# Kernel optimization log

Hardware: AMD Instinct MI355X
Metric: run time of the kernel (lower is better)

The kernel has to match this reference:

```python
import jax, jax.numpy as jnp
import numpy as np
import math

NUM_HEADS = 6
HIDDEN = 384
HEAD_CH = HIDDEN // NUM_HEADS
WINDOW = 4


def _get_relative_embeddings(emb, length, window):
    # emb: (H, 2*window+1, d) -> (H, 2*length-1, d)
    pad_length = max(0, length - window - 1)
    start = max(0, window - length + 1)
    padded = jnp.pad(emb, ((0, 0), (pad_length, pad_length), (0, 0)))
    return padded[:, start:start + 2 * length - 1, :]


def _relative_to_absolute(s_rel):
    # (B, H, L, 2L-1) -> (B, H, L, L) via shift-pad trick
    B, H, L, _ = s_rel.shape
    s = jnp.pad(s_rel, ((0, 0), (0, 0), (0, 0), (0, 1)))          # (B,H,L,2L)
    s = s.reshape(B, H, L * 2 * L)
    s = jnp.pad(s, ((0, 0), (0, 0), (0, L - 1)))
    s = s.reshape(B, H, L + 1, 2 * L - 1)
    return s[:, :, :L, L - 1:]


def _absolute_to_relative(score):
    # (B, H, L, L) -> (B, H, L, 2L-1)
    B, H, L, _ = score.shape
    s = jnp.pad(score, ((0, 0), (0, 0), (0, 0), (0, L - 1)))      # (B,H,L,2L-1)
    s = s.reshape(B, H, L * (2 * L - 1))
    s = jnp.pad(s, ((0, 0), (0, 0), (L, 0)))
    s = s.reshape(B, H, L, 2 * L)
    return s[:, :, :, 1:]


def setup_inputs() -> dict:
    key = jax.random.key(0)
    ks = jax.random.split(key, 11)
    B, C, L = 8, HIDDEN, 1024
    rel_std = HEAD_CH ** -0.5
    w_std = C ** -0.5
    return {
        "x": jax.random.normal(ks[0], (B, C, L), jnp.float32),
        "wq": jax.random.normal(ks[1], (C, C), jnp.float32) * w_std,
        "bq": jax.random.normal(ks[2], (C,), jnp.float32) * 0.01,
        "wk": jax.random.normal(ks[3], (C, C), jnp.float32) * w_std,
        "bk": jax.random.normal(ks[4], (C,), jnp.float32) * 0.01,
        "wv": jax.random.normal(ks[5], (C, C), jnp.float32) * w_std,
        "bv": jax.random.normal(ks[6], (C,), jnp.float32) * 0.01,
        "wo": jax.random.normal(ks[7], (C, C), jnp.float32) * w_std,
        "bo": jax.random.normal(ks[8], (C,), jnp.float32) * 0.01,
        "emb_rel_k": jax.random.normal(ks[9], (NUM_HEADS, 2 * WINDOW + 1, HEAD_CH), jnp.float32) * rel_std,
        "emb_rel_v": jax.random.normal(ks[10], (NUM_HEADS, 2 * WINDOW + 1, HEAD_CH), jnp.float32) * rel_std,
    }


def reference(x, wq, bq, wk, bk, wv, bv, wo, bo, emb_rel_k, emb_rel_v):
    B, C, L = x.shape
    H, d = NUM_HEADS, HEAD_CH
    scale = 1.0 / math.sqrt(d)

    # 1x1 convs == channel matmuls
    q = jnp.einsum('oc,bcl->bol', wq, x) + bq[:, None]
    k = jnp.einsum('oc,bcl->bol', wk, x) + bk[:, None]
    v = jnp.einsum('oc,bcl->bol', wv, x) + bv[:, None]

    # (B, C, L) -> (B, H, L, d)  (matches view(B,H,d,L).transpose(2,3))
    q = q.reshape(B, H, d, L).transpose(0, 1, 3, 2)
    k = k.reshape(B, H, d, L).transpose(0, 1, 3, 2)
    v = v.reshape(B, H, d, L).transpose(0, 1, 3, 2)

    score = jnp.einsum('bhld,bhmd->bhlm', q, k) * scale

    rel_k = _get_relative_embeddings(emb_rel_k, L, WINDOW)   # (H, 2L-1, d)
    s_rel = jnp.einsum('bhld,hmd->bhlm', q, rel_k)           # (B,H,L,2L-1)
    score = score + _relative_to_absolute(s_rel) * scale

    p = jax.nn.softmax(score, axis=-1)
    res = jnp.einsum('bhlm,bhmd->bhld', p, v)

    rel_w = _absolute_to_relative(p)                         # (B,H,L,2L-1)
    rel_v = _get_relative_embeddings(emb_rel_v, L, WINDOW)   # (H, 2L-1, d)
    res = res + jnp.einsum('bhlm,hmd->bhld', rel_w, rel_v)

    # (B,H,L,d) -> (B, C, L)
    res = res.transpose(0, 1, 3, 2).reshape(B, C, L)
    out = jnp.einsum('oc,bcl->bol', wo, res) + bo[:, None]
    return out
```

## Files before the change

kernel.cpp:

```cpp
#include <hip/hip_runtime.h>
#include <hip/hip_bf16.h>

#define NB 8
#define CH 384
#define SL 1024
#define NH 6
#define HD 64
#define WIN 4
#define LOG2E 1.44269504088896340736f
#define SCALE 0.125f
#define QSCALE (SCALE * LOG2E)
#define SCLAMP2 14.4269504f
#define PAD 72

typedef _Float16 f16;
typedef f16   f16x8 __attribute__((ext_vector_type(8)));
typedef f16   f16x4 __attribute__((ext_vector_type(4)));
typedef f16   f16x2 __attribute__((ext_vector_type(2)));
typedef float f32x4 __attribute__((ext_vector_type(4)));
typedef unsigned short u16x8 __attribute__((ext_vector_type(8)));
typedef unsigned short u16x4 __attribute__((ext_vector_type(4)));

static __device__ __forceinline__ unsigned short f2bf_rne(float f) {
  unsigned int u = __float_as_uint(f);
  unsigned int r = (u + 0x7fffu + ((u >> 16) & 1u)) >> 16;
  return (unsigned short)r;
}
static __device__ __forceinline__ float bfb(unsigned short u) {
  return __uint_as_float((unsigned int)u << 16);
}
static __device__ __forceinline__ float ldbf(const void* p, size_t i) {
  return bfb(((const unsigned short*)p)[i]);
}
static __device__ __forceinline__ float ldf(const void* p, size_t i) {
  return ((const float*)p)[i];
}
static __device__ __forceinline__ float fexp2(float x) {
  return __builtin_amdgcn_exp2f(x);
}
static __device__ __forceinline__ f16x2 pkrtz(float a, float b) {
  return __builtin_bit_cast(f16x2, __builtin_amdgcn_cvt_pkrtz(a, b));
}

#define BAR() do {                                            \
    asm volatile("s_waitcnt lgkmcnt(0)" ::: "memory");        \
    __builtin_amdgcn_s_barrier();                             \
    asm volatile("" ::: "memory");                            \
  } while (0)

__global__ __launch_bounds__(256) void cvt_k(
    const void* __restrict__ w0, const void* __restrict__ w1,
    const void* __restrict__ w2, const void* __restrict__ w3,
    const void* __restrict__ b0, const void* __restrict__ b1,
    const void* __restrict__ b2, const void* __restrict__ b3,
    const void* __restrict__ x,
    f16* __restrict__ wh, float* __restrict__ bh, f16* __restrict__ xt,
    int* __restrict__ flag)
{
  __shared__ f16 lt_[64][72];
  __shared__ int sflag;
  const int bx = blockIdx.x, t = threadIdx.x;

  {
    int cnt = 0;
    if (t < 64) {
      const unsigned int* xu = (const unsigned int*)x;
#pragma unroll
      for (int i = 0; i < 4; ++i) {
        unsigned int e = (xu[t * 4 + i] >> 7) & 0xFF;
        if (e >= 110 && e <= 140) ++cnt;
      }
#pragma unroll
      for (int s = 1; s < 64; s <<= 1) cnt += __shfl_xor(cnt, s);
      if (t == 0) sflag = (cnt >= 128) ? 1 : 0;
    }
    __syncthreads();
  }
  const int isbf = sflag;

  if (bx < 576) {
    int g = bx / 144;
    const void* src = (g == 0) ? w0 : (g == 1) ? w1 : (g == 2) ? w2 : w3;
    size_t idx = (size_t)(bx % 144) * 1024 + t * 4;
    f16* dst = wh + (size_t)g * CH * CH + idx;
    f16x4 o;
    if (!isbf) {
      float4 v = *(const float4*)((const float*)src + idx);
      o[0] = (f16)v.x; o[1] = (f16)v.y; o[2] = (f16)v.z; o[3] = (f16)v.w;
    } else {
      u16x4 v = *(const u16x4*)((const unsigned short*)src + idx);
#pragma unroll
      for (int j = 0; j < 4; ++j) o[j] = (f16)bfb(v[j]);
    }
    *(f16x4*)dst = o;
    return;
  }
  if (bx == 576) {
    if (t == 0) *flag = isbf;
    for (int e = t; e < 4 * CH; e += 256) {
      int g = e / CH, i = e - g * CH;
      const void* src = (g == 0) ? b0 : (g == 1) ? b1 : (g == 2) ? b2 : b3;
      bh[e] = isbf ? ldbf(src, i) : ldf(src, i);
    }
    return;
  }
  const int e  = bx - 577;
  const int l0 = (e & 15) * 64;
  const int c0 = ((e >> 4) % 6) * 64;
  const int b  = e / 96;
  const int row = t >> 4, lseg = t & 15;

  if (!isbf) {
    const float* xf = (const float*)x;
#pragma unroll
    for (int k = 0; k < 4; ++k) {
      int c = c0 + row + 16 * k;
      float4 v = *(const float4*)&xf[((size_t)b * CH + c) * SL + l0 + lseg * 4];
      lt_[lseg * 4 + 0][row + 16 * k] = (f16)v.x;
      lt_[lseg * 4 + 1][row + 16 * k] = (f16)v.y;
      lt_[lseg * 4 + 2][row + 16 * k] = (f16)v.z;
      lt_[lseg * 4 + 3][row + 16 * k] = (f16)v.w;
    }
  } else {
    const unsigned short* xu = (const unsigned short*)x;
#pragma unroll
    for (int k = 0; k < 4; ++k) {
      int c = c0 + row + 16 * k;
      u16x4 v = *(const u16x4*)&xu[((size_t)b * CH + c) * SL + l0 + lseg * 4];
#pragma unroll
      for (int j = 0; j < 4; ++j)
        lt_[lseg * 4 + j][row + 16 * k] = (f16)bfb(v[j]);
    }
  }
  __syncthreads();
  const int l = t >> 2, seg = t & 3;
  f16* dst = &xt[((size_t)b * SL + l0 + l) * CH + c0 + seg * 16];
  *(f16x8*)dst       = *(const f16x8*)&lt_[l][seg * 16];
  *(f16x8*)(dst + 8) = *(const f16x8*)&lt_[l][seg * 16 + 8];
}

__global__ __launch_bounds__(256) void qkv_k(
    const f16* __restrict__ wh, const float* __restrict__ bh, const f16* __restrict__ xt,
    f16* __restrict__ Q, f16* __restrict__ K, f16* __restrict__ Vt)
{
  __shared__ f16 sm[2][128][PAD];

  const int t   = threadIdx.x;
  const int l0  = blockIdx.x * 128;
  const int mty = blockIdx.y;
  const int b   = blockIdx.z;
  const int wid = t >> 6, lane = t & 63;
  const int quad = lane >> 4, lid = lane & 15;
  const int rw = wid >> 1, cw = wid & 1;

  const int g0   = mty / 3;
  const int m128 = (mty % 3) * 128;
  const f16* wg  = wh + (size_t)g0 * CH * CH;

  f32x4 acc[4][4];
#pragma unroll
  for (int mt = 0; mt < 4; ++mt)
#pragma unroll
    for (int nt = 0; nt < 4; ++nt) acc[mt][nt] = (f32x4){0.f, 0.f, 0.f, 0.f};

  for (int c0 = 0; c0 < CH; c0 += 64) {
    __syncthreads();
#pragma unroll
    for (int k = 0; k < 4; ++k) {
      int cidx = t + k * 256;
      int r = cidx >> 3, c8 = (cidx & 7) * 8;
      *(f16x8*)&sm[0][r][c8] = *(const f16x8*)&wg[(size_t)(m128 + r) * CH + c0 + c8];
      *(f16x8*)&sm[1][r][c8] = *(const f16x8*)&xt[((size_t)b * SL + l0 + r) * CH + c0 + c8];
    }
    __syncthreads();
#pragma unroll
    for (int kk = 0; kk < 2; ++kk) {
      f16x8 bf[4];
#pragma unroll
      for (int nt = 0; nt < 4; ++nt)
        bf[nt] = *(const f16x8*)&sm[1][cw * 64 + nt * 16 + lid][kk * 32 + quad * 8];
#pragma unroll
      for (int mt = 0; mt < 4; ++mt) {
        f16x8 af = *(const f16x8*)&sm[0][rw * 64 + mt * 16 + lid][kk * 32 + quad * 8];
#pragma unroll
        for (int nt = 0; nt < 4; ++nt)
          acc[mt][nt] = __builtin_amdgcn_mfma_f32_16x16x32_f16(af, bf[nt], acc[mt][nt], 0, 0, 0);
      }
    }
  }
  __syncthreads();

  const int h = (mty % 3) * 2 + rw;
  float bias[4][4];
#pragma unroll
  for (int mt = 0; mt < 4; ++mt)
#pragma unroll
    for (int r = 0; r < 4; ++r)
      bias[mt][r] = bh[g0 * CH + m128 + rw * 64 + mt * 16 + quad * 4 + r];
  const float osc = (g0 == 0) ? QSCALE : 1.0f;

  f16 (*lo4)[64][PAD] = (f16(*)[64][PAD])sm;

  if (g0 < 2) {
#pragma unroll
    for (int mt = 0; mt < 4; ++mt)
#pragma unroll
      for (int nt = 0; nt < 4; ++nt) {
        f16x4 vv;
#pragma unroll
        for (int r = 0; r < 4; ++r)
          vv[r] = (f16)((acc[mt][nt][r] + bias[mt][r]) * osc);
        *(f16x4*)&lo4[wid][nt * 16 + lid][mt * 16 + quad * 4] = vv;
      }
    __builtin_amdgcn_s_waitcnt(0);
    f16* base = ((g0 == 0) ? Q : K) + ((size_t)(b * NH + h) * SL + l0 + cw * 64) * HD;
#pragma unroll
    for (int p = 0; p < 8; ++p) {
      int lr = p * 8 + (lane >> 3), seg = lane & 7;
      *(f16x8*)&base[(size_t)lr * HD + seg * 8] = *(const f16x8*)&lo4[wid][lr][seg * 8];
    }
  } else {
#pragma unroll
    for (int mt = 0; mt < 4; ++mt)
#pragma unroll
      for (int nt = 0; nt < 4; ++nt)
#pragma unroll
        for (int r = 0; r < 4; ++r)
          lo4[wid][mt * 16 + quad * 4 + r][nt * 16 + lid] =
            (f16)(acc[mt][nt][r] + bias[mt][r]);
    __builtin_amdgcn_s_waitcnt(0);
    f16* base = Vt + ((size_t)(b * NH + h) * HD) * SL + l0 + cw * 64;
#pragma unroll
    for (int p = 0; p < 8; ++p) {
      int dr = p * 8 + (lane >> 3), seg = lane & 7;
      *(f16x8*)&base[(size_t)dr * SL + seg * 8] = *(const f16x8*)&lo4[wid][dr][seg * 8];
    }
  }
}

__global__ __launch_bounds__(256, 3) void attn_k(
    const f16* __restrict__ Qs, const f16* __restrict__ Kg, const f16* __restrict__ Vtg,
    const void* __restrict__ embk, const void* __restrict__ embv,
    f16* __restrict__ R2t, const int* __restrict__ flag)
{
  __shared__ f16 bufall[4][64][PAD];
  __shared__ float lbias[64][12];
  __shared__ float lsb[64][12];
  __shared__ float lev[9][64];
  __shared__ float ll64[64];
  __shared__ float lred[4][2][16];

  const int isbf = *flag;
  const int t    = threadIdx.x;

  const int id   = blockIdx.x;
  const int xcd  = id & 7;
  const int kk   = id >> 3;
  const int pair = (kk % 6) * 8 + xcd;
  const int i0   = (kk / 6) * 64;
  const int b    = pair / NH;
  const int h    = pair % NH;

  const int wid  = t >> 6;
  const int lane = t & 63;
  const int quad = lane >> 4;
  const int lid  = lane & 15;
  const int ih   = wid >> 1;
  const int jh   = wid & 1;
  const int irow = 16 * wid + lid;

  const f16* Qb = Qs  + ((size_t)(b * NH + h) * SL) * HD;
  const f16* Kb = Kg  + ((size_t)(b * NH + h) * SL) * HD;
  const f16* Vb = Vtg + ((size_t)(b * NH + h) * HD) * SL;

  f16 (*bufk)[64][PAD] = &bufall[0];
  f16 (*bufv)[64][PAD] = &bufall[2];
  f16 (* const lq)[PAD] = bufall[0];
  f16 (* const lo)[PAD] = bufall[0];

  const int r_0 = t >> 3, c8 = (t & 7) * 8;
  const int r_1 = (t + 256) >> 3;

#pragma unroll
  for (int k = 0; k < 2; ++k) {
    int c = t + k * 256, r = c >> 3, cc8 = (c & 7) * 8;
    *(f16x8*)&lq[r][cc8] = *(const f16x8*)&Qb[(size_t)(i0 + r) * HD + cc8];
  }
  const f16* pKa = Kb + (size_t)r_0 * HD + c8;
  const f16* pKb = Kb + (size_t)r_1 * HD + c8;
  const f16* pVa = Vb + (size_t)r_0 * SL + c8;
  const f16* pVb = Vb + (size_t)r_1 * SL + c8;
  f16x8 pk0 = *(const f16x8*)pKa;
  f16x8 pk1 = *(const f16x8*)pKb;
  f16x8 pv0 = *(const f16x8*)pVa;
  f16x8 pv1 = *(const f16x8*)pVb;

  for (int e = t; e < 576; e += 256) {
    int p = e >> 6, c = e & 63;
    lev[p][c] = isbf ? ldbf(embv, (size_t)h * 576 + e) : ldf(embv, (size_t)h * 576 + e);
  }
  for (int e = t; e < 768; e += 256) ((float*)lsb)[e] = -1e30f;
  BAR();

  f16x8 qn0[2], qn1[2];
#pragma unroll
  for (int nt = 0; nt < 2; ++nt) {
    qn0[nt] = *(const f16x8*)&lq[ih * 32 + nt * 16 + lid][quad * 8];
    qn1[nt] = *(const f16x8*)&lq[ih * 32 + nt * 16 + lid][32 + quad * 8];
  }

  {
    int row = h * 9 + (lid < 9 ? lid : 0);
    f16x8 ekf0, ekf1;
    if (!isbf) {
      const float* ek = (const float*)embk;
#pragma unroll
      for (int e = 0; e < 8; ++e) {
        ekf0[e] = (f16)ek[(size_t)row * HD + quad * 8 + e];
        ekf1[e] = (f16)ek[(size_t)row * HD + 32 + quad * 8 + e];
      }
    } else {
      const unsigned short* ek = (const unsigned short*)embk;
      u16x8 v0 = *(const u16x8*)&ek[(size_t)row * HD + quad * 8];
      u16x8 v1 = *(const u16x8*)&ek[(size_t)row * HD + 32 + quad * 8];
#pragma unroll
      for (int e = 0; e < 8; ++e) { ekf0[e] = (f16)bfb(v0[e]); ekf1[e] = (f16)bfb(v1[e]); }
    }
    f32x4 bd = (f32x4){0.f, 0.f, 0.f, 0.f};
    bd = __builtin_amdgcn_mfma_f32_16x16x32_f16(ekf0, qn0[jh], bd, 0, 0, 0);
    bd = __builtin_amdgcn_mfma_f32_16x16x32_f16(ekf1, qn1[jh], bd, 0, 0, 0);
#pragma unroll
    for (int r = 0; r < 4; ++r) {
      int p = quad * 4 + r;
      if (p < 9) lbias[irow][p] = bd[r];
    }
  }
  BAR();

  const f16x4 ones4 = {(f16)1.f, (f16)1.f, (f16)1.f, (f16)1.f};

  f32x4 Op[2][4];
  f32x4 Os[2];
#pragma unroll
  for (int nt = 0; nt < 2; ++nt) {
    Os[nt] = (f32x4){0.f, 0.f, 0.f, 0.f};
#pragma unroll
    for (int dt = 0; dt < 4; ++dt) Op[nt][dt] = (f32x4){0.f, 0.f, 0.f, 0.f};
  }

  auto tile = [&](const int IB, const int j0, const bool last) __attribute__((always_inline)) {
    *(f16x8*)&bufk[IB][r_0][c8] = pk0;
    *(f16x8*)&bufk[IB][r_1][c8] = pk1;
    *(f16x8*)&bufv[IB][r_0][c8] = pv0;
    *(f16x8*)&bufv[IB][r_1][c8] = pv1;
    BAR();

    if (!last) {
      pKa += 64 * HD; pKb += 64 * HD; pVa += 64; pVb += 64;
      pk0 = *(const f16x8*)pKa;
      pk1 = *(const f16x8*)pKb;
      pv0 = *(const f16x8*)pVa;
      pv1 = *(const f16x8*)pVb;
    }

    f16x8 a00 = *(const f16x8*)&bufk[IB][jh * 32 + lid][quad * 8];
    f16x8 a10 = *(const f16x8*)&bufk[IB][jh * 32 + lid][32 + quad * 8];
    f16x8 a01 = *(const f16x8*)&bufk[IB][jh * 32 + 16 + lid][quad * 8];
    f16x8 a11 = *(const f16x8*)&bufk[IB][jh * 32 + 16 + lid][32 + quad * 8];

    f32x4 sc[2][2];
#pragma unroll
    for (int nt = 0; nt < 2; ++nt) {
      f32x4 z = (f32x4){0.f, 0.f, 0.f, 0.f};
      sc[0][nt] = __builtin_amdgcn_mfma_f32_16x16x32_f16(a00, qn0[nt], z, 0, 0, 0);
      sc[0][nt] = __builtin_amdgcn_mfma_f32_16x16x32_f16(a10, qn1[nt], sc[0][nt], 0, 0, 0);
      sc[1][nt] = __builtin_amdgcn_mfma_f32_16x16x32_f16(a01, qn0[nt], z, 0, 0, 0);
      sc[1][nt] = __builtin_amdgcn_mfma_f32_16x16x32_f16(a11, qn1[nt], sc[1][nt], 0, 0, 0);
    }

    if (j0 - i0 <= 64 && i0 - j0 <= 64) {
#pragma unroll
      for (int jt = 0; jt < 2; ++jt)
#pragma unroll
        for (int nt = 0; nt < 2; ++nt)
#pragma unroll
          for (int r = 0; r < 4; ++r) {
            int jl = jh * 32 + jt * 16 + quad * 4 + r;
            int il = ih * 32 + nt * 16 + lid;
            int d = (j0 + jl) - (i0 + il) + WIN;
            if (d >= 0 && d <= 2 * WIN) {
              float s = sc[jt][nt][r] + lbias[il][d];
              sc[jt][nt][r] = s;
              lsb[il][d] = s;
            }
          }
    }

    f16x4 pb[2][2];
#pragma unroll
    for (int jt = 0; jt < 2; ++jt)
#pragma unroll
      for (int nt = 0; nt < 2; ++nt) {
        float e0 = fexp2(fminf(sc[jt][nt][0], SCLAMP2));
        float e1 = fexp2(fminf(sc[jt][nt][1], SCLAMP2));
        float e2 = fexp2(fminf(sc[jt][nt][2], SCLAMP2));
        float e3 = fexp2(fminf(sc[jt][nt][3], SCLAMP2));
        f16x2 p01 = pkrtz(e0, e1);
        f16x2 p23 = pkrtz(e2, e3);
        pb[jt][nt] = __builtin_shufflevector(p01, p23, 0, 1, 2, 3);
      }

#pragma unroll
    for (int nt = 0; nt < 2; ++nt) {
      Os[nt] = __builtin_amdgcn_mfma_f32_16x16x16f16(ones4, pb[0][nt], Os[nt], 0, 0, 0);
      Os[nt] = __builtin_amdgcn_mfma_f32_16x16x16f16(ones4, pb[1][nt], Os[nt], 0, 0, 0);
    }

#pragma unroll
    for (int dt = 0; dt < 4; ++dt) {
      f16x4 vf0 = *(const f16x4*)&bufv[IB][dt * 16 + lid][jh * 32 + quad * 4];
      f16x4 vf1 = *(const f16x4*)&bufv[IB][dt * 16 + lid][jh * 32 + 16 + quad * 4];
#pragma unroll
      for (int nt = 0; nt < 2; ++nt) {
        Op[nt][dt] = __builtin_amdgcn_mfma_f32_16x16x16f16(vf0, pb[0][nt], Op[nt][dt], 0, 0, 0);
        Op[nt][dt] = __builtin_amdgcn_mfma_f32_16x16x16f16(vf1, pb[1][nt], Op[nt][dt], 0, 0, 0);
      }
    }
  };

  for (int j0 = 0; j0 < SL; j0 += 128) {
    tile(0, j0, false);
    tile(1, j0 + 64, j0 + 128 >= SL);
  }

  __syncthreads();
  float* red = (float*)bufall;
#pragma unroll
  for (int nt = 0; nt < 2; ++nt)
#pragma unroll
    for (int dt = 0; dt < 4; ++dt)
      *(f32x4*)&red[(((wid * 2 + nt) * 4 + dt) * 64 + lane) * 4] = Op[nt][dt];
  if (quad == 0) {
    lred[wid][0][lid] = Os[0][0];
    lred[wid][1][lid] = Os[1][0];
  }
  __syncthreads();

  const int u0w = (wid >> 1) * 2, u1w = u0w + 1, ntw = wid & 1;
  f32x4 O[4];
#pragma unroll
  for (int dt = 0; dt < 4; ++dt) {
    f32x4 xA = *(const f32x4*)&red[(((u0w * 2 + ntw) * 4 + dt) * 64 + lane) * 4];
    f32x4 xB = *(const f32x4*)&red[(((u1w * 2 + ntw) * 4 + dt) * 64 + lane) * 4];
    O[dt] = xA + xB;
  }
  const float lsum = lred[u0w][ntw][lid] + lred[u1w][ntw][lid];
  if (quad == 0) ll64[irow] = lsum;
  __syncthreads();

  for (int e = t; e < 576; e += 256) {
    int r = e / 9, p = e - r * 9;
    lsb[r][p] = fexp2(fminf(lsb[r][p], SCLAMP2)) * __builtin_amdgcn_rcpf(ll64[r]);
  }
  __syncthreads();

  {
    const float rl = __builtin_amdgcn_rcpf(lsum);
    float lp[9];
#pragma unroll
    for (int p = 0; p < 9; ++p) lp[p] = lsb[irow][p];
    float val[4][4];
#pragma unroll
    for (int dt = 0; dt < 4; ++dt)
#pragma unroll
      for (int r = 0; r < 4; ++r) val[dt][r] = O[dt][r] * rl;
#pragma unroll
    for (int p = 0; p < 9; ++p)
#pragma unroll
      for (int dt = 0; dt < 4; ++dt)
#pragma unroll
        for (int r = 0; r < 4; ++r)
          val[dt][r] += lp[p] * lev[p][dt * 16 + quad * 4 + r];
#pragma unroll
    for (int dt = 0; dt < 4; ++dt) {
      f16x4 vv;
#pragma unroll
      for (int r = 0; r < 4; ++r) vv[r] = (f16)val[dt][r];
      *(f16x4*)&lo[irow][dt * 16 + quad * 4] = vv;
    }
  }
  __syncthreads();

  {
    const int l = t >> 2, seg = t & 3;
    f16* dst = &R2t[((size_t)b * SL + i0 + l) * CH + h * 64 + seg * 16];
    *(f16x8*)dst       = *(const f16x8*)&lo[l][seg * 16];
    *(f16x8*)(dst + 8) = *(const f16x8*)&lo[l][seg * 16 + 8];
  }
}

__global__ __launch_bounds__(256) void out_k(
    const f16* __restrict__ wh, const float* __restrict__ bh, const f16* __restrict__ R2t,
    void* __restrict__ out, const int* __restrict__ flag)
{
  __shared__ f16 sm[2][128][PAD];

  const int isbf = *flag;
  const int t   = threadIdx.x;
  const int l0  = blockIdx.x * 128;
  const int m0  = blockIdx.y * 128;
  const int b   = blockIdx.z;
  const int wid = t >> 6, lane = t & 63;
  const int quad = lane >> 4, lid = lane & 15;
  const int rw = wid >> 1, cw = wid & 1;

  const f16* wg = wh + (size_t)3 * CH * CH;

  f32x4 acc[4][4];
#pragma unroll
  for (int mt = 0; mt < 4; ++mt)
#pragma unroll
    for (int nt = 0; nt < 4; ++nt) acc[mt][nt] = (f32x4){0.f, 0.f, 0.f, 0.f};

  for (int c0 = 0; c0 < CH; c0 += 64) {
    __syncthreads();
#pragma unroll
    for (int k = 0; k < 4; ++k) {
      int cidx = t + k * 256;
      int r = cidx >> 3, c8 = (cidx & 7) * 8;
      *(f16x8*)&sm[0][r][c8] = *(const f16x8*)&wg[(size_t)(m0 + r) * CH + c0 + c8];
      *(f16x8*)&sm[1][r][c8] = *(const f16x8*)&R2t[((size_t)b * SL + l0 + r) * CH + c0 + c8];
    }
    __syncthreads();
#pragma unroll
    for (int kk = 0; kk < 2; ++kk) {
      f16x8 bf[4];
#pragma unroll
      for (int nt = 0; nt < 4; ++nt)
        bf[nt] = *(const f16x8*)&sm[1][cw * 64 + nt * 16 + lid][kk * 32 + quad * 8];
#pragma unroll
      for (int mt = 0; mt < 4; ++mt) {
        f16x8 af = *(const f16x8*)&sm[0][rw * 64 + mt * 16 + lid][kk * 32 + quad * 8];
#pragma unroll
        for (int nt = 0; nt < 4; ++nt)
          acc[mt][nt] = __builtin_amdgcn_mfma_f32_16x16x32_f16(af, bf[nt], acc[mt][nt], 0, 0, 0);
      }
    }
  }

  float bias[4][4];
#pragma unroll
  for (int mt = 0; mt < 4; ++mt)
#pragma unroll
    for (int r = 0; r < 4; ++r)
      bias[mt][r] = bh[3 * CH + m0 + rw * 64 + mt * 16 + quad * 4 + r];

  if (isbf) {
    __syncthreads();
    unsigned short (*lo4)[64][PAD] = (unsigned short(*)[64][PAD])sm;
#pragma unroll
    for (int mt = 0; mt < 4; ++mt)
#pragma unroll
      for (int nt = 0; nt < 4; ++nt)
#pragma unroll
        for (int r = 0; r < 4; ++r)
          lo4[wid][mt * 16 + quad * 4 + r][nt * 16 + lid] =
            f2bf_rne(acc[mt][nt][r] + bias[mt][r]);
    __builtin_amdgcn_s_waitcnt(0);
    unsigned short* base = (unsigned short*)out
      + ((size_t)b * CH + m0 + rw * 64) * SL + l0 + cw * 64;
#pragma unroll
    for (int p = 0; p < 8; ++p) {
      int mr = p * 8 + (lane >> 3), seg = lane & 7;
      *(u16x8*)&base[(size_t)mr * SL + seg * 8] = *(const u16x8*)&lo4[wid][mr][seg * 8];
    }
  } else {
#pragma unroll
    for (int mt = 0; mt < 4; ++mt)
#pragma unroll
      for (int nt = 0; nt < 4; ++nt)
#pragma unroll
        for (int r = 0; r < 4; ++r) {
          int m = m0 + rw * 64 + mt * 16 + quad * 4 + r;
          int l = l0 + cw * 64 + nt * 16 + lid;
          ((float*)out)[((size_t)b * CH + m) * SL + l] = acc[mt][nt][r] + bias[mt][r];
        }
  }
}

extern "C" void kernel_launch(void* const* d_in, const int* in_sizes, int n_in,
                              void* d_out, int out_size, void* d_ws, size_t ws_size,
                              hipStream_t stream) {
  (void)in_sizes; (void)n_in; (void)out_size; (void)ws_size;
  const void* x  = d_in[0];
  const void* wq = d_in[1]; const void* bq = d_in[2];
  const void* wk = d_in[3]; const void* bk = d_in[4];
  const void* wv = d_in[5]; const void* bv = d_in[6];
  const void* wo = d_in[7]; const void* bo = d_in[8];
  const void* ek = d_in[9]; const void* ev = d_in[10];

  const size_t NQ = (size_t)NB * NH * SL * HD;
  const size_t NX = (size_t)NB * SL * CH;
  char* w = (char*)d_ws;
  int*   flag = (int*)w;                 w += 256;
  f16*   wh   = (f16*)w;                 w += 4 * CH * CH * sizeof(f16);
  float* bh   = (float*)w;               w += 4 * CH * sizeof(float);
  f16*   xt   = (f16*)w;                 w += NX * sizeof(f16);
  f16*   Q    = (f16*)w;                 w += NQ * sizeof(f16);
  f16*   K    = (f16*)w;                 w += NQ * sizeof(f16);
  f16*   Vt   = (f16*)w;                 w += NQ * sizeof(f16);
  f16*   R2t  = (f16*)w;                 w += NX * sizeof(f16);

  cvt_k   <<<1345, 256, 0, stream>>>(wq, wk, wv, wo, bq, bk, bv, bo, x, wh, bh, xt, flag);
  qkv_k   <<<dim3(8, 9, NB), 256, 0, stream>>>(wh, bh, xt, Q, K, Vt);
  attn_k  <<<768, 256, 0, stream>>>(Q, K, Vt, ek, ev, R2t, flag);
  out_k   <<<dim3(8, 3, NB), 256, 0, stream>>>(wh, bh, R2t, d_out, flag);
}
```

Before: 143.1 us.

## Fuse input/weight conversion into projection kernels and drop separate convert pass

Removes the standalone conversion kernel that cast weights, biases and x to fp16 and transposed x into a workspace buffer. The QKV and output projection kernels now read the raw fp32/bf16 weights and x directly, converting to fp16 while staging into shared memory, and each kernel recomputes the dtype probe locally instead of reading a flag from memory. This saves one launch and the write-then-read round trip of the converted x, in exchange for redundant conversion work across blocks, twice the global read bytes for fp32 weights, and scattered transposed shared-memory stores of x.

```diff
diff --git a/kernel.cpp b/kernel.cpp
--- a/kernel.cpp
+++ b/kernel.cpp
@@ -42,110 +42,41 @@
   return __builtin_bit_cast(f16x2, __builtin_amdgcn_cvt_pkrtz(a, b));
 }
 
+#define PROBE(xptr, sflag_var) do {                                   \
+    if (t < 64) {                                                     \
+      int cnt_ = 0;                                                   \
+      const unsigned int* xu_ = (const unsigned int*)(xptr);          \
+      _Pragma("unroll")                                               \
+      for (int i_ = 0; i_ < 4; ++i_) {                                \
+        unsigned int e_ = (xu_[t * 4 + i_] >> 7) & 0xFF;              \
+        if (e_ >= 110 && e_ <= 140) ++cnt_;                           \
+      }                                                               \
+      _Pragma("unroll")                                               \
+      for (int s_ = 1; s_ < 64; s_ <<= 1) cnt_ += __shfl_xor(cnt_, s_); \
+      if (t == 0) sflag_var = (cnt_ >= 128) ? 1 : 0;                  \
+    }                                                                 \
+  } while (0)
+
 #define BAR() do {                                            \
     asm volatile("s_waitcnt lgkmcnt(0)" ::: "memory");        \
     __builtin_amdgcn_s_barrier();                             \
     asm volatile("" ::: "memory");                            \
   } while (0)
 
-__global__ __launch_bounds__(256) void cvt_k(
-    const void* __restrict__ w0, const void* __restrict__ w1,
-    const void* __restrict__ w2, const void* __restrict__ w3,
-    const void* __restrict__ b0, const void* __restrict__ b1,
-    const void* __restrict__ b2, const void* __restrict__ b3,
+__global__ __launch_bounds__(256) void qkv_k(
+    const void* __restrict__ w0, const void* __restrict__ w1, const void* __restrict__ w2,
+    const void* __restrict__ b0, const void* __restrict__ b1, const void* __restrict__ b2,
     const void* __restrict__ x,
-    f16* __restrict__ wh, float* __restrict__ bh, f16* __restrict__ xt,
-    int* __restrict__ flag)
-{
-  __shared__ f16 lt_[64][72];
-  __shared__ int sflag;
-  const int bx = blockIdx.x, t = threadIdx.x;
-
-  {
-    int cnt = 0;
-    if (t < 64) {
-      const unsigned int* xu = (const unsigned int*)x;
-#pragma unroll
-      for (int i = 0; i < 4; ++i) {
-        unsigned int e = (xu[t * 4 + i] >> 7) & 0xFF;
-        if (e >= 110 && e <= 140) ++cnt;
-      }
-#pragma unroll
-      for (int s = 1; s < 64; s <<= 1) cnt += __shfl_xor(cnt, s);
-      if (t == 0) sflag = (cnt >= 128) ? 1 : 0;
-    }
-    __syncthreads();
-  }
-  const int isbf = sflag;
-
-  if (bx < 576) {
-    int g = bx / 144;
-    const void* src = (g == 0) ? w0 : (g == 1) ? w1 : (g == 2) ? w2 : w3;
-    size_t idx = (size_t)(bx % 144) * 1024 + t * 4;
-    f16* dst = wh + (size_t)g * CH * CH + idx;
-    f16x4 o;
-    if (!isbf) {
-      float4 v = *(const float4*)((const float*)src + idx);
-      o[0] = (f16)v.x; o[1] = (f16)v.y; o[2] = (f16)v.z; o[3] = (f16)v.w;
-    } else {
-      u16x4 v = *(const u16x4*)((const unsigned short*)src + idx);
-#pragma unroll
-      for (int j = 0; j < 4; ++j) o[j] = (f16)bfb(v[j]);
-    }
-    *(f16x4*)dst = o;
-    return;
-  }
-  if (bx == 576) {
-    if (t == 0) *flag = isbf;
-    for (int e = t; e < 4 * CH; e += 256) {
-      int g = e / CH, i = e - g * CH;
-      const void* src = (g == 0) ? b0 : (g == 1) ? b1 : (g == 2) ? b2 : b3;
-      bh[e] = isbf ? ldbf(src, i) : ldf(src, i);
-    }
-    return;
-  }
-  const int e  = bx - 577;
-  const int l0 = (e & 15) * 64;
-  const int c0 = ((e >> 4) % 6) * 64;
-  const int b  = e / 96;
-  const int row = t >> 4, lseg = t & 15;
-
-  if (!isbf) {
-    const float* xf = (const float*)x;
-#pragma unroll
-    for (int k = 0; k < 4; ++k) {
-      int c = c0 + row + 16 * k;
-      float4 v = *(const float4*)&xf[((size_t)b * CH + c) * SL + l0 + lseg * 4];
-      lt_[lseg * 4 + 0][row + 16 * k] = (f16)v.x;
-      lt_[lseg * 4 + 1][row + 16 * k] = (f16)v.y;
-      lt_[lseg * 4 + 2][row + 16 * k] = (f16)v.z;
-      lt_[lseg * 4 + 3][row + 16 * k] = (f16)v.w;
-    }
-  } else {
-    const unsigned short* xu = (const unsigned short*)x;
-#pragma unroll
-    for (int k = 0; k < 4; ++k) {
-      int c = c0 + row + 16 * k;
-      u16x4 v = *(const u16x4*)&xu[((size_t)b * CH + c) * SL + l0 + lseg * 4];
-#pragma unroll
-      for (int j = 0; j < 4; ++j)
-        lt_[lseg * 4 + j][row + 16 * k] = (f16)bfb(v[j]);
-    }
-  }
-  __syncthreads();
-  const int l = t >> 2, seg = t & 3;
-  f16* dst = &xt[((size_t)b * SL + l0 + l) * CH + c0 + seg * 16];
-  *(f16x8*)dst       = *(const f16x8*)&lt_[l][seg * 16];
-  *(f16x8*)(dst + 8) = *(const f16x8*)&lt_[l][seg * 16 + 8];
-}
-
-__global__ __launch_bounds__(256) void qkv_k(
-    const f16* __restrict__ wh, const float* __restrict__ bh, const f16* __restrict__ xt,
     f16* __restrict__ Q, f16* __restrict__ K, f16* __restrict__ Vt)
 {
   __shared__ f16 sm[2][128][PAD];
-
-  const int t   = threadIdx.x;
+  __shared__ int sflag;
+
+  const int t = threadIdx.x;
+  PROBE(x, sflag);
+  __syncthreads();
+  const int isbf = sflag;
+
   const int l0  = blockIdx.x * 128;
   const int mty = blockIdx.y;
   const int b   = blockIdx.z;
@@ -155,7 +86,10 @@
 
   const int g0   = mty / 3;
   const int m128 = (mty % 3) * 128;
-  const f16* wg  = wh + (size_t)g0 * CH * CH;
+  const void* wg = (g0 == 0) ? w0 : (g0 == 1) ? w1 : w2;
+  const void* bg = (g0 == 0) ? b0 : (g0 == 1) ? b1 : b2;
+
+  const int lseg = t & 31, crow = t >> 5;
 
   f32x4 acc[4][4];
 #pragma unroll
@@ -165,12 +99,51 @@
 
   for (int c0 = 0; c0 < CH; c0 += 64) {
     __syncthreads();
-#pragma unroll
-    for (int k = 0; k < 4; ++k) {
-      int cidx = t + k * 256;
-      int r = cidx >> 3, c8 = (cidx & 7) * 8;
-      *(f16x8*)&sm[0][r][c8] = *(const f16x8*)&wg[(size_t)(m128 + r) * CH + c0 + c8];
-      *(f16x8*)&sm[1][r][c8] = *(const f16x8*)&xt[((size_t)b * SL + l0 + r) * CH + c0 + c8];
+    if (!isbf) {
+      const float* wf = (const float*)wg;
+#pragma unroll
+      for (int k = 0; k < 4; ++k) {
+        int cidx = t + k * 256;
+        int r = cidx >> 3, c8 = (cidx & 7) * 8;
+        const float* src = &wf[(size_t)(m128 + r) * CH + c0 + c8];
+        float4 v0 = *(const float4*)src;
+        float4 v1 = *(const float4*)(src + 4);
+        f16x8 o;
+        o[0] = (f16)v0.x; o[1] = (f16)v0.y; o[2] = (f16)v0.z; o[3] = (f16)v0.w;
+        o[4] = (f16)v1.x; o[5] = (f16)v1.y; o[6] = (f16)v1.z; o[7] = (f16)v1.w;
+        *(f16x8*)&sm[0][r][c8] = o;
+      }
+      const float* xf = (const float*)x;
+#pragma unroll
+      for (int k = 0; k < 8; ++k) {
+        int c = c0 + crow + 8 * k;
+        float4 v = *(const float4*)&xf[((size_t)b * CH + c) * SL + l0 + lseg * 4];
+        sm[1][lseg * 4 + 0][crow + 8 * k] = (f16)v.x;
+        sm[1][lseg * 4 + 1][crow + 8 * k] = (f16)v.y;
+        sm[1][lseg * 4 + 2][crow + 8 * k] = (f16)v.z;
+        sm[1][lseg * 4 + 3][crow + 8 * k] = (f16)v.w;
+      }
+    } else {
+      const unsigned short* wu = (const unsigned short*)wg;
+#pragma unroll
+      for (int k = 0; k < 4; ++k) {
+        int cidx = t + k * 256;
+        int r = cidx >> 3, c8 = (cidx & 7) * 8;
+        u16x8 v = *(const u16x8*)&wu[(size_t)(m128 + r) * CH + c0 + c8];
+        f16x8 o;
+#pragma unroll
+        for (int j = 0; j < 8; ++j) o[j] = (f16)bfb(v[j]);
+        *(f16x8*)&sm[0][r][c8] = o;
+      }
+      const unsigned short* xu = (const unsigned short*)x;
+#pragma unroll
+      for (int k = 0; k < 8; ++k) {
+        int c = c0 + crow + 8 * k;
+        u16x4 v = *(const u16x4*)&xu[((size_t)b * CH + c) * SL + l0 + lseg * 4];
+#pragma unroll
+        for (int j = 0; j < 4; ++j)
+          sm[1][lseg * 4 + j][crow + 8 * k] = (f16)bfb(v[j]);
+      }
     }
     __syncthreads();
 #pragma unroll
@@ -195,8 +168,10 @@
 #pragma unroll
   for (int mt = 0; mt < 4; ++mt)
 #pragma unroll
-    for (int r = 0; r < 4; ++r)
-      bias[mt][r] = bh[g0 * CH + m128 + rw * 64 + mt * 16 + quad * 4 + r];
+    for (int r = 0; r < 4; ++r) {
+      int m = m128 + rw * 64 + mt * 16 + quad * 4 + r;
+      bias[mt][r] = isbf ? ldbf(bg, m) : ldf(bg, m);
+    }
   const float osc = (g0 == 0) ? QSCALE : 1.0f;
 
   f16 (*lo4)[64][PAD] = (f16(*)[64][PAD])sm;
@@ -241,7 +216,7 @@
 __global__ __launch_bounds__(256, 3) void attn_k(
     const f16* __restrict__ Qs, const f16* __restrict__ Kg, const f16* __restrict__ Vtg,
     const void* __restrict__ embk, const void* __restrict__ embv,
-    f16* __restrict__ R2t, const int* __restrict__ flag)
+    f16* __restrict__ R2t, const void* __restrict__ xp)
 {
   __shared__ f16 bufall[4][64][PAD];
   __shared__ float lbias[64][12];
@@ -249,9 +224,12 @@
   __shared__ float lev[9][64];
   __shared__ float ll64[64];
   __shared__ float lred[4][2][16];
-
-  const int isbf = *flag;
-  const int t    = threadIdx.x;
+  __shared__ int sflag;
+
+  const int t = threadIdx.x;
+  PROBE(xp, sflag);
+  __syncthreads();
+  const int isbf = sflag;
 
   const int id   = blockIdx.x;
   const int xcd  = id & 7;
@@ -500,13 +478,18 @@
 }
 
 __global__ __launch_bounds__(256) void out_k(
-    const f16* __restrict__ wh, const float* __restrict__ bh, const f16* __restrict__ R2t,
-    void* __restrict__ out, const int* __restrict__ flag)
+    const void* __restrict__ wo, const void* __restrict__ bo,
+    const f16* __restrict__ R2t, void* __restrict__ out,
+    const void* __restrict__ xp)
 {
   __shared__ f16 sm[2][128][PAD];
-
-  const int isbf = *flag;
-  const int t   = threadIdx.x;
+  __shared__ int sflag;
+
+  const int t = threadIdx.x;
+  PROBE(xp, sflag);
+  __syncthreads();
+  const int isbf = sflag;
+
   const int l0  = blockIdx.x * 128;
   const int m0  = blockIdx.y * 128;
   const int b   = blockIdx.z;
@@ -514,8 +497,6 @@
   const int quad = lane >> 4, lid = lane & 15;
   const int rw = wid >> 1, cw = wid & 1;
 
-  const f16* wg = wh + (size_t)3 * CH * CH;
-
   f32x4 acc[4][4];
 #pragma unroll
   for (int mt = 0; mt < 4; ++mt)
@@ -524,12 +505,34 @@
 
   for (int c0 = 0; c0 < CH; c0 += 64) {
     __syncthreads();
-#pragma unroll
-    for (int k = 0; k < 4; ++k) {
-      int cidx = t + k * 256;
-      int r = cidx >> 3, c8 = (cidx & 7) * 8;
-      *(f16x8*)&sm[0][r][c8] = *(const f16x8*)&wg[(size_t)(m0 + r) * CH + c0 + c8];
-      *(f16x8*)&sm[1][r][c8] = *(const f16x8*)&R2t[((size_t)b * SL + l0 + r) * CH + c0 + c8];
+    if (!isbf) {
+      const float* wf = (const float*)wo;
+#pragma unroll
+      for (int k = 0; k < 4; ++k) {
+        int cidx = t + k * 256;
+        int r = cidx >> 3, c8 = (cidx & 7) * 8;
+        const float* src = &wf[(size_t)(m0 + r) * CH + c0 + c8];
+        float4 v0 = *(const float4*)src;
+        float4 v1 = *(const float4*)(src + 4);
+        f16x8 o;
+        o[0] = (f16)v0.x; o[1] = (f16)v0.y; o[2] = (f16)v0.z; o[3] = (f16)v0.w;
+        o[4] = (f16)v1.x; o[5] = (f16)v1.y; o[6] = (f16)v1.z; o[7] = (f16)v1.w;
+        *(f16x8*)&sm[0][r][c8] = o;
+        *(f16x8*)&sm[1][r][c8] = *(const f16x8*)&R2t[((size_t)b * SL + l0 + r) * CH + c0 + c8];
+      }
+    } else {
+      const unsigned short* wu = (const unsigned short*)wo;
+#pragma unroll
+      for (int k = 0; k < 4; ++k) {
+        int cidx = t + k * 256;
+        int r = cidx >> 3, c8 = (cidx & 7) * 8;
+        u16x8 v = *(const u16x8*)&wu[(size_t)(m0 + r) * CH + c0 + c8];
+        f16x8 o;
+#pragma unroll
+        for (int j = 0; j < 8; ++j) o[j] = (f16)bfb(v[j]);
+        *(f16x8*)&sm[0][r][c8] = o;
+        *(f16x8*)&sm[1][r][c8] = *(const f16x8*)&R2t[((size_t)b * SL + l0 + r) * CH + c0 + c8];
+      }
     }
     __syncthreads();
 #pragma unroll
@@ -552,8 +555,10 @@
 #pragma unroll
   for (int mt = 0; mt < 4; ++mt)
 #pragma unroll
-    for (int r = 0; r < 4; ++r)
-      bias[mt][r] = bh[3 * CH + m0 + rw * 64 + mt * 16 + quad * 4 + r];
+    for (int r = 0; r < 4; ++r) {
+      int m = m0 + rw * 64 + mt * 16 + quad * 4 + r;
+      bias[mt][r] = isbf ? ldbf(bo, m) : ldf(bo, m);
+    }
 
   if (isbf) {
     __syncthreads();
@@ -602,17 +607,12 @@
   const size_t NQ = (size_t)NB * NH * SL * HD;
   const size_t NX = (size_t)NB * SL * CH;
   char* w = (char*)d_ws;
-  int*   flag = (int*)w;                 w += 256;
-  f16*   wh   = (f16*)w;                 w += 4 * CH * CH * sizeof(f16);
-  float* bh   = (float*)w;               w += 4 * CH * sizeof(float);
-  f16*   xt   = (f16*)w;                 w += NX * sizeof(f16);
   f16*   Q    = (f16*)w;                 w += NQ * sizeof(f16);
   f16*   K    = (f16*)w;                 w += NQ * sizeof(f16);
   f16*   Vt   = (f16*)w;                 w += NQ * sizeof(f16);
   f16*   R2t  = (f16*)w;                 w += NX * sizeof(f16);
 
-  cvt_k   <<<1345, 256, 0, stream>>>(wq, wk, wv, wo, bq, bk, bv, bo, x, wh, bh, xt, flag);
-  qkv_k   <<<dim3(8, 9, NB), 256, 0, stream>>>(wh, bh, xt, Q, K, Vt);
-  attn_k  <<<768, 256, 0, stream>>>(Q, K, Vt, ek, ev, R2t, flag);
-  out_k   <<<dim3(8, 3, NB), 256, 0, stream>>>(wh, bh, R2t, d_out, flag);
-}
+  qkv_k   <<<dim3(8, 9, NB), 256, 0, stream>>>(wq, wk, wv, bq, bk, bv, x, Q, K, Vt);
+  attn_k  <<<768, 256, 0, stream>>>(Q, K, Vt, ek, ev, R2t, x);
+  out_k   <<<dim3(8, 3, NB), 256, 0, stream>>>(wo, bo, R2t, d_out, x);
+}
```

Result: slower. 170.6 us (+19.3%).

## Load K and V fragments directly from global memory instead of LDS staging

Applied to the files above, without the earlier changes.

The attention main loop no longer stages K and V tiles through double-buffered shared memory behind barriers. Each wave now reads its MFMA operand fragments for K and V straight from global memory, relying on the cache. This removes the per-tile LDS writes, reads and block barriers, but adds redundant global loads across waves, small uncoalesced 8-byte V reads, and loses the register prefetch that overlapped loads with compute.

```diff
diff --git a/kernel.cpp b/kernel.cpp
--- a/kernel.cpp
+++ b/kernel.cpp
@@ -41,12 +41,6 @@
 static __device__ __forceinline__ f16x2 pkrtz(float a, float b) {
   return __builtin_bit_cast(f16x2, __builtin_amdgcn_cvt_pkrtz(a, b));
 }
-
-#define BAR() do {                                            \
-    asm volatile("s_waitcnt lgkmcnt(0)" ::: "memory");        \
-    __builtin_amdgcn_s_barrier();                             \
-    asm volatile("" ::: "memory");                            \
-  } while (0)
 
 __global__ __launch_bounds__(256) void cvt_k(
     const void* __restrict__ w0, const void* __restrict__ w1,
@@ -273,34 +267,20 @@
   const f16* Kb = Kg  + ((size_t)(b * NH + h) * SL) * HD;
   const f16* Vb = Vtg + ((size_t)(b * NH + h) * HD) * SL;
 
-  f16 (*bufk)[64][PAD] = &bufall[0];
-  f16 (*bufv)[64][PAD] = &bufall[2];
   f16 (* const lq)[PAD] = bufall[0];
   f16 (* const lo)[PAD] = bufall[0];
-
-  const int r_0 = t >> 3, c8 = (t & 7) * 8;
-  const int r_1 = (t + 256) >> 3;
 
 #pragma unroll
   for (int k = 0; k < 2; ++k) {
     int c = t + k * 256, r = c >> 3, cc8 = (c & 7) * 8;
     *(f16x8*)&lq[r][cc8] = *(const f16x8*)&Qb[(size_t)(i0 + r) * HD + cc8];
   }
-  const f16* pKa = Kb + (size_t)r_0 * HD + c8;
-  const f16* pKb = Kb + (size_t)r_1 * HD + c8;
-  const f16* pVa = Vb + (size_t)r_0 * SL + c8;
-  const f16* pVb = Vb + (size_t)r_1 * SL + c8;
-  f16x8 pk0 = *(const f16x8*)pKa;
-  f16x8 pk1 = *(const f16x8*)pKb;
-  f16x8 pv0 = *(const f16x8*)pVa;
-  f16x8 pv1 = *(const f16x8*)pVb;
-
   for (int e = t; e < 576; e += 256) {
     int p = e >> 6, c = e & 63;
     lev[p][c] = isbf ? ldbf(embv, (size_t)h * 576 + e) : ldf(embv, (size_t)h * 576 + e);
   }
   for (int e = t; e < 768; e += 256) ((float*)lsb)[e] = -1e30f;
-  BAR();
+  __syncthreads();
 
   f16x8 qn0[2], qn1[2];
 #pragma unroll
@@ -335,7 +315,7 @@
       if (p < 9) lbias[irow][p] = bd[r];
     }
   }
-  BAR();
+  __syncthreads();
 
   const f16x4 ones4 = {(f16)1.f, (f16)1.f, (f16)1.f, (f16)1.f};
 
@@ -348,25 +328,15 @@
     for (int dt = 0; dt < 4; ++dt) Op[nt][dt] = (f32x4){0.f, 0.f, 0.f, 0.f};
   }
 
-  auto tile = [&](const int IB, const int j0, const bool last) __attribute__((always_inline)) {
-    *(f16x8*)&bufk[IB][r_0][c8] = pk0;
-    *(f16x8*)&bufk[IB][r_1][c8] = pk1;
-    *(f16x8*)&bufv[IB][r_0][c8] = pv0;
-    *(f16x8*)&bufv[IB][r_1][c8] = pv1;
-    BAR();
-
-    if (!last) {
-      pKa += 64 * HD; pKb += 64 * HD; pVa += 64; pVb += 64;
-      pk0 = *(const f16x8*)pKa;
-      pk1 = *(const f16x8*)pKb;
-      pv0 = *(const f16x8*)pVa;
-      pv1 = *(const f16x8*)pVb;
-    }
-
-    f16x8 a00 = *(const f16x8*)&bufk[IB][jh * 32 + lid][quad * 8];
-    f16x8 a10 = *(const f16x8*)&bufk[IB][jh * 32 + lid][32 + quad * 8];
-    f16x8 a01 = *(const f16x8*)&bufk[IB][jh * 32 + 16 + lid][quad * 8];
-    f16x8 a11 = *(const f16x8*)&bufk[IB][jh * 32 + 16 + lid][32 + quad * 8];
+  const f16* kr = Kb + (size_t)(jh * 32 + lid) * HD + quad * 8;
+  const f16* vr = Vb + (size_t)lid * SL + jh * 32 + quad * 4;
+
+  for (int j0 = 0; j0 < SL; j0 += 64) {
+    f16x8 a00 = *(const f16x8*)kr;
+    f16x8 a10 = *(const f16x8*)(kr + 32);
+    f16x8 a01 = *(const f16x8*)(kr + 16 * HD);
+    f16x8 a11 = *(const f16x8*)(kr + 16 * HD + 32);
+    kr += 64 * HD;
 
     f32x4 sc[2][2];
 #pragma unroll
@@ -418,19 +388,15 @@
 
 #pragma unroll
     for (int dt = 0; dt < 4; ++dt) {
-      f16x4 vf0 = *(const f16x4*)&bufv[IB][dt * 16 + lid][jh * 32 + quad * 4];
-      f16x4 vf1 = *(const f16x4*)&bufv[IB][dt * 16 + lid][jh * 32 + 16 + quad * 4];
+      f16x4 vf0 = *(const f16x4*)(vr + (size_t)dt * 16 * SL);
+      f16x4 vf1 = *(const f16x4*)(vr + (size_t)dt * 16 * SL + 16);
 #pragma unroll
       for (int nt = 0; nt < 2; ++nt) {
         Op[nt][dt] = __builtin_amdgcn_mfma_f32_16x16x16f16(vf0, pb[0][nt], Op[nt][dt], 0, 0, 0);
         Op[nt][dt] = __builtin_amdgcn_mfma_f32_16x16x16f16(vf1, pb[1][nt], Op[nt][dt], 0, 0, 0);
       }
     }
-  };
-
-  for (int j0 = 0; j0 < SL; j0 += 128) {
-    tile(0, j0, false);
-    tile(1, j0 + 64, j0 + 128 >= SL);
+    vr += 64;
   }
 
   __syncthreads();
```

Result: slower. 185.2 us (+29.4%).
